# Kernel optimization log

Measured on AMD Instinct MI355X. Metric: run time of the kernel, lower is better.

## Reference

```python
import jax, jax.numpy as jnp
import numpy as np

B, T, D = 2, 2048, 1024
H = 16
HD = D // H  # 64


def _rope_tables(t_len, hd, dtype=jnp.float32):
    inv_freq = 1.0 / (10000.0 ** (jnp.arange(0, hd, 2, dtype=jnp.float32) / hd))
    freqs = jnp.outer(jnp.arange(t_len, dtype=jnp.float32), inv_freq)  # [T, hd/2]
    emb = jnp.concatenate([freqs, freqs], axis=-1)  # [T, hd]
    return emb.astype(dtype)


def _rotate_half(x):
    x1, x2 = jnp.split(x, 2, axis=-1)
    return jnp.concatenate([-x2, x1], axis=-1)


def setup_inputs() -> dict:
    key = jax.random.key(0)
    k1, k2, k3 = jax.random.split(key, 3)
    x = jax.random.normal(k1, (B, T, D), dtype=jnp.float32)
    w_qkv = jax.random.normal(k2, (D, 3 * D), dtype=jnp.float32) * (D ** -0.5)
    w_out = jax.random.normal(k3, (D, D), dtype=jnp.float32) * (D ** -0.5)
    return {"x": x, "w_qkv": w_qkv, "w_out": w_out}


def reference(x, w_qkv, w_out):
    Bc, Tc, Dc = x.shape
    scale = HD ** -0.5
    qkv = x @ w_qkv  # [B,T,3D]
    q, k, v = jnp.split(qkv, 3, axis=-1)
    # -> [B,H,T,hd]
    q = q.reshape(Bc, Tc, H, HD).transpose(0, 2, 1, 3)
    k = k.reshape(Bc, Tc, H, HD).transpose(0, 2, 1, 3)
    v = v.reshape(Bc, Tc, H, HD).transpose(0, 2, 1, 3)
    emb = _rope_tables(Tc, HD, x.dtype)  # [T,hd]
    cos = jnp.cos(emb)[None, None, :, :]
    sin = jnp.sin(emb)[None, None, :, :]
    q = q * cos + _rotate_half(q) * sin
    k = k * cos + _rotate_half(k) * sin
    attn = jnp.einsum('bhqd,bhkd->bhqk', q, k) * scale  # [B,H,T,T]
    causal = jnp.tril(jnp.ones((Tc, Tc), dtype=bool))
    attn = jnp.where(causal[None, None], attn, -jnp.inf)
    attn = jax.nn.softmax(attn, axis=-1)
    out = jnp.einsum('bhqk,bhkd->bhqd', attn, v)
    out = out.transpose(0, 2, 1, 3).reshape(Bc, Tc, Dc)
    return out @ w_out
```

## Files before the change

### kernel.cpp

```cpp
#include <hip/hip_runtime.h>

#define TSEQ 2048
#define DMODEL 1024
#define NHEAD 16
#define HDIM 64
#define NB 2
#define MROWS 4096
#define NQKV 3072
#define QSCALE 0.1803368801111204f
#define ROPE_C (13.2877123795494f / 32.0f)
#define NEGINF -3.0e38f

using s16x8 = __attribute__((ext_vector_type(8))) short;
using s16x4 = __attribute__((ext_vector_type(4))) short;
using f32x4 = __attribute__((ext_vector_type(4))) float;
using u32x2 = __attribute__((ext_vector_type(2))) unsigned int;

static __device__ __forceinline__ float b2f(unsigned short u) {
  union { unsigned int i; float f; } x; x.i = ((unsigned int)u) << 16; return x.f;
}
static __device__ __forceinline__ unsigned short f2b(float f) {
  unsigned int u = __float_as_uint(f);
  u += 0x7fffu + ((u >> 16) & 1u);
  return (unsigned short)(u >> 16);
}

typedef const __attribute__((address_space(1))) char gchar;
typedef __attribute__((address_space(3))) char lchar;
static __device__ __forceinline__ void gload_lds16(const void* g, void* l) {
  __builtin_amdgcn_global_load_lds((gchar*)g, (lchar*)l, 16, 0, 0);
}

__global__ __launch_bounds__(256) void k_prep(const float* __restrict__ x,
                                              short* __restrict__ xb,
                                              const float* __restrict__ wq,
                                              short* __restrict__ wqT,
                                              const float* __restrict__ wo,
                                              short* __restrict__ woT) {
  __shared__ float tile[32][33];
  const int blk = blockIdx.x;
  const int tid = threadIdx.x;
  if (blk < 4096) {
    const int i = blk * 256 + tid;
    const float4 v = ((const float4*)x)[i];
    s16x4 o;
    o.x = (short)f2b(v.x); o.y = (short)f2b(v.y);
    o.z = (short)f2b(v.z); o.w = (short)f2b(v.w);
    ((s16x4*)xb)[i] = o;
    return;
  }
  const float* in; short* out; int C, bx, by;
  if (blk < 7168) {
    const int l = blk - 4096; in = wq; out = wqT; C = NQKV;
    bx = l % 96; by = l / 96;
  } else {
    const int l = blk - 7168; in = wo; out = woT; C = DMODEL;
    bx = l & 31; by = l >> 5;
  }
  const int tx = tid & 31, ty4 = (tid >> 5) * 4;
#pragma unroll
  for (int i = 0; i < 4; ++i)
    tile[ty4 + i][tx] = in[(by * 32 + ty4 + i) * C + bx * 32 + tx];
  __syncthreads();
#pragma unroll
  for (int i = 0; i < 4; ++i)
    out[(bx * 32 + ty4 + i) * DMODEL + by * 32 + tx] = (short)f2b(tile[tx][ty4 + i]);
}

__global__ __launch_bounds__(256) void k_gemm_qkv(const short* __restrict__ A,
                                                  const short* __restrict__ BT,
                                                  short* __restrict__ Qo,
                                                  short* __restrict__ Ko,
                                                  short* __restrict__ Vt) {
  __shared__ __attribute__((aligned(16))) short As[128 * 64];
  __shared__ __attribute__((aligned(16))) short Bs[128 * 64];
  const int K = DMODEL;
  const int tid = threadIdx.x;
  const int wave = tid >> 6, lane = tid & 63, quad = lane >> 4, l15 = lane & 15;
  const int wm = (wave >> 1) * 64, wn = (wave & 1) * 64;
  const int m0 = blockIdx.y * 128, n0 = blockIdx.x * 128;
  f32x4 acc[4][4] = {};
  const char* Ab = (const char*)A;
  const char* Bb = (const char*)BT;
  char* AsB = (char*)As;
  char* BsB = (char*)Bs;
  int srow[4], sg[4];
#pragma unroll
  for (int p = 0; p < 4; ++p) {
    const int i = p * 256 + tid;
    srow[p] = i >> 3;
    sg[p] = (i & 7) ^ (srow[p] & 7);
  }
  for (int k0 = 0; k0 < K; k0 += 64) {
    __syncthreads();
#pragma unroll
    for (int p = 0; p < 4; ++p) {
      const long go = ((long)(m0 + srow[p]) * K + k0) * 2 + sg[p] * 16;
      gload_lds16(Ab + go, AsB + p * 4096 + wave * 1024);
    }
#pragma unroll
    for (int p = 0; p < 4; ++p) {
      const long go = ((long)(n0 + srow[p]) * K + k0) * 2 + sg[p] * 16;
      gload_lds16(Bb + go, BsB + p * 4096 + wave * 1024);
    }
    __syncthreads();
#pragma unroll
    for (int hf = 0; hf < 2; ++hf) {
      s16x8 af[4], bf[4];
#pragma unroll
      for (int i = 0; i < 4; ++i) {
        const int ra = wm + i * 16 + l15;
        af[i] = *(const s16x8*)(AsB + ra * 128 + (((hf * 4 + quad) ^ (ra & 7)) * 16));
        const int rb = wn + i * 16 + l15;
        bf[i] = *(const s16x8*)(BsB + rb * 128 + (((hf * 4 + quad) ^ (rb & 7)) * 16));
      }
#pragma unroll
      for (int i = 0; i < 4; ++i)
#pragma unroll
        for (int j = 0; j < 4; ++j)
          acc[i][j] = __builtin_amdgcn_mfma_f32_16x16x32_bf16(af[i], bf[j], acc[i][j], 0, 0, 0);
    }
  }
  const int colbase = n0 + wn;
  const int region = colbase >> 10;
  const int hh = (colbase & 1023) >> 6;
  const int bq = m0 >> 11;
  const int tbase = (m0 & 2047) + wm;
  if (region == 2) {
    short* dst = Vt + (((long)(bq * NHEAD + hh) * HDIM) << 11);
#pragma unroll
    for (int i = 0; i < 4; ++i) {
      const int t0 = tbase + i * 16 + quad * 4;
#pragma unroll
      for (int j = 0; j < 4; ++j) {
        const int d = j * 16 + l15;
        s16x4 w;
        w.x = (short)f2b(acc[i][j][0]);
        w.y = (short)f2b(acc[i][j][1]);
        w.z = (short)f2b(acc[i][j][2]);
        w.w = (short)f2b(acc[i][j][3]);
        *(s16x4*)(dst + (((long)d) << 11) + t0) = w;
      }
    }
  } else {
    short* dst = (region ? Ko : Qo) + (long)(bq * NHEAD + hh) * TSEQ * HDIM;
#pragma unroll
    for (int i = 0; i < 4; ++i)
#pragma unroll
      for (int j = 0; j < 4; ++j) {
        const int d = j * 16 + l15;
#pragma unroll
        for (int r = 0; r < 4; ++r) {
          const int t = tbase + i * 16 + quad * 4 + r;
          dst[(long)t * HDIM + d] = (short)f2b(acc[i][j][r]);
        }
      }
  }
}

__global__ __launch_bounds__(256) void k_ropek(short* __restrict__ Kp) {
  const int tt = blockIdx.x, bh = blockIdx.y;
  const int tid = threadIdx.x;
  const int row = tid >> 2, chunk = tid & 3;
  const int t = tt * 64 + row;
  short* base = Kp + ((long)bh * TSEQ + t) * HDIM + chunk * 8;
  const s16x8 lo = *(const s16x8*)base;
  const s16x8 hi = *(const s16x8*)(base + 32);
  s16x8 nlo, nhi;
  const float tf = (float)t;
#pragma unroll
  for (int j = 0; j < 8; ++j) {
    const float inv = exp2f(-(float)(chunk * 8 + j) * ROPE_C);
    float sn, cs;
    __sincosf(tf * inv, &sn, &cs);
    const float a = b2f((unsigned short)lo[j]);
    const float b = b2f((unsigned short)hi[j]);
    nlo[j] = (short)f2b(a * cs - b * sn);
    nhi[j] = (short)f2b(b * cs + a * sn);
  }
  *(s16x8*)base = nlo;
  *(s16x8*)(base + 32) = nhi;
}

template <int IM, bool OUT_BF16>
__global__ __launch_bounds__(256) void k_gemm(const short* __restrict__ A,
                                              const short* __restrict__ BT,
                                              void* __restrict__ Cv,
                                              int M, int N, int K) {
  __shared__ __attribute__((aligned(16))) short As[IM * 32 * 64];
  __shared__ __attribute__((aligned(16))) short Bs[128 * 64];
  const int tid = threadIdx.x;
  const int wave = tid >> 6, lane = tid & 63, quad = lane >> 4, l15 = lane & 15;
  const int wm = (wave >> 1) * (IM * 16), wn = (wave & 1) * 64;
  const int m0 = blockIdx.y * (IM * 32), n0 = blockIdx.x * 128;
  f32x4 acc[IM][4] = {};
  const char* Ab = (const char*)A;
  const char* Bb = (const char*)BT;
  char* AsB = (char*)As;
  char* BsB = (char*)Bs;
  int srow[4], sg[4];
#pragma unroll
  for (int p = 0; p < 4; ++p) {
    const int i = p * 256 + tid;
    srow[p] = i >> 3;
    sg[p] = (i & 7) ^ (srow[p] & 7);
  }
  for (int k0 = 0; k0 < K; k0 += 64) {
    __syncthreads();
#pragma unroll
    for (int p = 0; p < IM; ++p) {
      const long go = ((long)(m0 + srow[p]) * K + k0) * 2 + sg[p] * 16;
      gload_lds16(Ab + go, AsB + p * 4096 + wave * 1024);
    }
#pragma unroll
    for (int p = 0; p < 4; ++p) {
      const long go = ((long)(n0 + srow[p]) * K + k0) * 2 + sg[p] * 16;
      gload_lds16(Bb + go, BsB + p * 4096 + wave * 1024);
    }
    __syncthreads();
#pragma unroll
    for (int hf = 0; hf < 2; ++hf) {
      s16x8 af[IM], bf[4];
#pragma unroll
      for (int i = 0; i < IM; ++i) {
        const int ra = wm + i * 16 + l15;
        af[i] = *(const s16x8*)(AsB + ra * 128 + (((hf * 4 + quad) ^ (ra & 7)) * 16));
      }
#pragma unroll
      for (int j = 0; j < 4; ++j) {
        const int rb = wn + j * 16 + l15;
        bf[j] = *(const s16x8*)(BsB + rb * 128 + (((hf * 4 + quad) ^ (rb & 7)) * 16));
      }
#pragma unroll
      for (int i = 0; i < IM; ++i)
#pragma unroll
        for (int j = 0; j < 4; ++j)
          acc[i][j] = __builtin_amdgcn_mfma_f32_16x16x32_bf16(af[i], bf[j], acc[i][j], 0, 0, 0);
    }
  }
#pragma unroll
  for (int i = 0; i < IM; ++i) {
    const int row = m0 + wm + i * 16 + quad * 4;
#pragma unroll
    for (int j = 0; j < 4; ++j) {
      const int col = n0 + wn + j * 16 + l15;
#pragma unroll
      for (int r = 0; r < 4; ++r) {
        if (OUT_BF16) ((short*)Cv)[(long)(row + r) * N + col] = (short)f2b(acc[i][j][r]);
        else          ((float*)Cv)[(long)(row + r) * N + col] = acc[i][j][r];
      }
    }
  }
}

__global__ __launch_bounds__(512) __attribute__((amdgpu_waves_per_eu(4)))
void k_attn(const short* __restrict__ Qg,
            const short* __restrict__ Kg,
            const short* __restrict__ Vg,
            short* __restrict__ O) {
  __shared__ __attribute__((aligned(16))) short Ks[2][64 * 64];
  __shared__ __attribute__((aligned(16))) short Vs[2][64 * 64];
  __shared__ __attribute__((aligned(16))) short pl[8][16 * 64];
  const int bx = blockIdx.x, by = blockIdx.y;
  const int qi = ((by >> 4) & 1) ? (15 - bx) : bx;
  const int bh = by;
  const int b = bh >> 4, h = bh & 15;
  const int tid = threadIdx.x, wave = tid >> 6, lane = tid & 63;
  const int quad = lane >> 4, l15 = lane & 15;
  const char* Kb = (const char*)(Kg + (long)bh * TSEQ * HDIM);
  const char* Vb = (const char*)(Vg + (long)bh * HDIM * TSEQ);
  const short* Qb = Qg + (long)bh * TSEQ * HDIM;
  const int qr0 = qi * 128 + wave * 16;
  const s16x8 rq0 = *(const s16x8*)&Qb[(qr0 + l15) * HDIM + quad * 8];
  const s16x8 rq1 = *(const s16x8*)&Qb[(qr0 + l15) * HDIM + 32 + quad * 8];
  s16x8 aq0, aq1;
  {
    const float tf = (float)(qr0 + l15);
#pragma unroll
    for (int j = 0; j < 8; ++j) {
      const float inv = exp2f(-(float)(quad * 8 + j) * ROPE_C);
      float sn, cs;
      __sincosf(tf * inv, &sn, &cs);
      sn *= QSCALE; cs *= QSCALE;
      const float q0 = b2f((unsigned short)rq0[j]);
      const float q1 = b2f((unsigned short)rq1[j]);
      aq0[j] = (short)f2b(q0 * cs - q1 * sn);
      aq1[j] = (short)f2b(q1 * cs + q0 * sn);
    }
  }
  f32x4 o[4] = {};
  float lsum = 0.0f;
  const int kr0 = tid >> 3, kg0 = (tid & 7) ^ (kr0 & 7);
  char* KsB = (char*)Ks;
  char* VsB = (char*)Vs;
  char* plwB = (char*)pl + wave * 2048;
  const int ldsw = wave * 1024;

#define STAGE(kjv, buf)                                                     \
  do {                                                                      \
    gload_lds16(Kb + (kjv) * 8192 + (kr0 * 8 + kg0) * 16,                   \
                KsB + (buf) * 8192 + ldsw);                                 \
    gload_lds16(Vb + (kjv) * 128 + kr0 * (TSEQ * 2) + kg0 * 16,             \
                VsB + (buf) * 8192 + ldsw);                                 \
  } while (0)

  STAGE(0, 0);
  __syncthreads();

  const int kjmax = 2 * qi + 1;
  const int kjd = qr0 >> 6;
  for (int kj = 0; kj <= kjmax; ++kj) {
    const int cur = kj & 1;
    if (kj < kjmax) STAGE(kj + 1, cur ^ 1);
    if (kj <= kjd) {
      const char* kb = KsB + cur * 8192;
      const char* vb = VsB + cur * 8192;
      f32x4 s[4];
#pragma unroll
      for (int j2 = 0; j2 < 4; ++j2) {
        const int row = j2 * 16 + l15;
        const s16x8 k0 = *(const s16x8*)(kb + row * 128 + ((quad ^ (row & 7)) * 16));
        const s16x8 k1 = *(const s16x8*)(kb + row * 128 + (((4 + quad) ^ (row & 7)) * 16));
        f32x4 z = {};
        z = __builtin_amdgcn_mfma_f32_16x16x32_bf16(k0, aq0, z, 0, 0, 0);
        z = __builtin_amdgcn_mfma_f32_16x16x32_bf16(k1, aq1, z, 0, 0, 0);
        s[j2] = z;
      }
      if (kj == kjd) {
        const int qloc = (qr0 & 63) + l15;
#pragma unroll
        for (int j2 = 0; j2 < 4; ++j2)
#pragma unroll
          for (int r = 0; r < 4; ++r)
            if (j2 * 16 + quad * 4 + r > qloc) s[j2][r] = NEGINF;
      }
      float ps = 0.0f;
#pragma unroll
      for (int j2 = 0; j2 < 4; ++j2) {
        const unsigned int u0 = __float_as_uint(exp2f(s[j2][0])) & 0xffff0000u;
        const unsigned int u1 = __float_as_uint(exp2f(s[j2][1])) & 0xffff0000u;
        const unsigned int u2 = __float_as_uint(exp2f(s[j2][2])) & 0xffff0000u;
        const unsigned int u3 = __float_as_uint(exp2f(s[j2][3])) & 0xffff0000u;
        ps += __uint_as_float(u0) + __uint_as_float(u1) +
              __uint_as_float(u2) + __uint_as_float(u3);
        u32x2 w;
        w.x = (u0 >> 16) | u1;
        w.y = (u2 >> 16) | u3;
        const int t0 = j2 * 16 + quad * 4;
        *(u32x2*)(plwB + l15 * 128 + (((t0 >> 3) ^ (l15 & 7)) * 16) + (quad & 1) * 8) = w;
      }
      lsum += ps;
      const s16x8 bp0 = *(const s16x8*)(plwB + l15 * 128 + ((quad ^ (l15 & 7)) * 16));
      const s16x8 bp1 = *(const s16x8*)(plwB + l15 * 128 + (((4 + quad) ^ (l15 & 7)) * 16));
#pragma unroll
      for (int hs = 0; hs < 4; ++hs) {
        const int d = hs * 16 + l15;
        const s16x8 av0 = *(const s16x8*)(vb + d * 128 + ((quad ^ (d & 7)) * 16));
        const s16x8 av1 = *(const s16x8*)(vb + d * 128 + (((4 + quad) ^ (d & 7)) * 16));
        o[hs] = __builtin_amdgcn_mfma_f32_16x16x32_bf16(av0, bp0, o[hs], 0, 0, 0);
        o[hs] = __builtin_amdgcn_mfma_f32_16x16x32_bf16(av1, bp1, o[hs], 0, 0, 0);
      }
    }
    __syncthreads();
  }
#undef STAGE
  lsum += __shfl_xor(lsum, 16);
  lsum += __shfl_xor(lsum, 32);
  const float rinv = 1.0f / lsum;
  const int t = qr0 + l15;
  short* Orow = O + (long)(b * TSEQ + t) * DMODEL + h * HDIM + quad * 4;
#pragma unroll
  for (int hs = 0; hs < 4; ++hs) {
    s16x4 w;
    w.x = (short)f2b(o[hs][0] * rinv);
    w.y = (short)f2b(o[hs][1] * rinv);
    w.z = (short)f2b(o[hs][2] * rinv);
    w.w = (short)f2b(o[hs][3] * rinv);
    *(s16x4*)(Orow + hs * 16) = w;
  }
}

extern "C" void kernel_launch(void* const* d_in, const int* in_sizes, int n_in,
                              void* d_out, int out_size, void* d_ws, size_t ws_size,
                              hipStream_t stream) {
  const float* x = (const float*)d_in[0];
  const float* w_qkv = (const float*)d_in[1];
  const float* w_out = (const float*)d_in[2];
  float* out = (float*)d_out;
  char* ws = (char*)d_ws;

  short* xb    = (short*)(ws);
  short* wqkvT = (short*)(ws + (8ll << 20));
  short* woutT = (short*)(ws + (14ll << 20));
  short* Qb    = (short*)(ws + (16ll << 20));
  short* Kb    = (short*)(ws + (24ll << 20));
  short* Vt    = (short*)(ws + (32ll << 20));
  short* Ob    = (short*)(ws + (40ll << 20));

  k_prep<<<dim3(8192), dim3(256), 0, stream>>>(x, xb, w_qkv, wqkvT, w_out, woutT);
  k_gemm_qkv<<<dim3(NQKV / 128, MROWS / 128), dim3(256), 0, stream>>>(
      xb, wqkvT, Qb, Kb, Vt);
  k_ropek<<<dim3(TSEQ / 64, NB * NHEAD), dim3(256), 0, stream>>>(Kb);
  k_attn<<<dim3(TSEQ / 128, NB * NHEAD), dim3(512), 0, stream>>>(Qb, Kb, Vt, Ob);
  k_gemm<2, false><<<dim3(DMODEL / 128, MROWS / 64), dim3(256), 0, stream>>>(
      Ob, woutT, (void*)out, MROWS, DMODEL, DMODEL);
}
```

Measured before the change: 192.5 us.

## Give each attention wave two 16-row query tiles and halve the block size

The attention kernel now runs 4 waves per block instead of 8, and each wave owns 32 query rows split into two 16-row subtiles. Each K and V fragment read from LDS feeds twice as many MFMAs, which cuts LDS read traffic per unit of work. The K/V tile staging is split across two loads per thread to match the smaller block. In exchange, register pressure roughly doubles for the accumulators (waves_per_eu lowered to 2). The causal skip is also coarser: a wave keeps processing key blocks up to the diagonal of its last row, which adds some wasted work for the first subtile.

```diff
diff --git a/kernel.cpp b/kernel.cpp
--- a/kernel.cpp
+++ b/kernel.cpp
@@ -253,14 +253,14 @@
   }
 }
 
-__global__ __launch_bounds__(512) __attribute__((amdgpu_waves_per_eu(4)))
+__global__ __launch_bounds__(256) __attribute__((amdgpu_waves_per_eu(2)))
 void k_attn(const short* __restrict__ Qg,
             const short* __restrict__ Kg,
             const short* __restrict__ Vg,
             short* __restrict__ O) {
   __shared__ __attribute__((aligned(16))) short Ks[2][64 * 64];
   __shared__ __attribute__((aligned(16))) short Vs[2][64 * 64];
-  __shared__ __attribute__((aligned(16))) short pl[8][16 * 64];
+  __shared__ __attribute__((aligned(16))) short pl[4][2][16 * 64];
   const int bx = blockIdx.x, by = blockIdx.y;
   const int qi = ((by >> 4) & 1) ? (15 - bx) : bx;
   const int bh = by;
@@ -270,12 +270,14 @@
   const char* Kb = (const char*)(Kg + (long)bh * TSEQ * HDIM);
   const char* Vb = (const char*)(Vg + (long)bh * HDIM * TSEQ);
   const short* Qb = Qg + (long)bh * TSEQ * HDIM;
-  const int qr0 = qi * 128 + wave * 16;
-  const s16x8 rq0 = *(const s16x8*)&Qb[(qr0 + l15) * HDIM + quad * 8];
-  const s16x8 rq1 = *(const s16x8*)&Qb[(qr0 + l15) * HDIM + 32 + quad * 8];
-  s16x8 aq0, aq1;
-  {
-    const float tf = (float)(qr0 + l15);
+  const int qw0 = qi * 128 + wave * 32;
+  s16x8 aq[2][2];
+#pragma unroll
+  for (int qh = 0; qh < 2; ++qh) {
+    const int qrow = qw0 + qh * 16 + l15;
+    const s16x8 rq0 = *(const s16x8*)&Qb[qrow * HDIM + quad * 8];
+    const s16x8 rq1 = *(const s16x8*)&Qb[qrow * HDIM + 32 + quad * 8];
+    const float tf = (float)qrow;
 #pragma unroll
     for (int j = 0; j < 8; ++j) {
       const float inv = exp2f(-(float)(quad * 8 + j) * ROPE_C);
@@ -284,99 +286,122 @@
       sn *= QSCALE; cs *= QSCALE;
       const float q0 = b2f((unsigned short)rq0[j]);
       const float q1 = b2f((unsigned short)rq1[j]);
-      aq0[j] = (short)f2b(q0 * cs - q1 * sn);
-      aq1[j] = (short)f2b(q1 * cs + q0 * sn);
-    }
-  }
-  f32x4 o[4] = {};
-  float lsum = 0.0f;
+      aq[qh][0][j] = (short)f2b(q0 * cs - q1 * sn);
+      aq[qh][1][j] = (short)f2b(q1 * cs + q0 * sn);
+    }
+  }
+  f32x4 o[2][4] = {};
+  float lsum[2] = {0.0f, 0.0f};
   const int kr0 = tid >> 3, kg0 = (tid & 7) ^ (kr0 & 7);
+  const int kr1 = (tid + 256) >> 3, kg1 = (tid & 7) ^ (kr1 & 7);
   char* KsB = (char*)Ks;
   char* VsB = (char*)Vs;
-  char* plwB = (char*)pl + wave * 2048;
-  const int ldsw = wave * 1024;
+  char* plwB = (char*)pl + wave * 4096;
+  const int ldsw0 = wave * 1024, ldsw1 = 4096 + wave * 1024;
 
 #define STAGE(kjv, buf)                                                     \
   do {                                                                      \
-    gload_lds16(Kb + (kjv) * 8192 + (kr0 * 8 + kg0) * 16,                   \
-                KsB + (buf) * 8192 + ldsw);                                 \
-    gload_lds16(Vb + (kjv) * 128 + kr0 * (TSEQ * 2) + kg0 * 16,             \
-                VsB + (buf) * 8192 + ldsw);                                 \
+    const char* Kt_ = Kb + (kjv) * 8192;                                    \
+    const char* Vt_ = Vb + (kjv) * 128;                                     \
+    char* kd_ = KsB + (buf) * 8192;                                         \
+    char* vd_ = VsB + (buf) * 8192;                                         \
+    gload_lds16(Kt_ + (kr0 * 8 + kg0) * 16, kd_ + ldsw0);                   \
+    gload_lds16(Kt_ + (kr1 * 8 + kg1) * 16, kd_ + ldsw1);                   \
+    gload_lds16(Vt_ + kr0 * (TSEQ * 2) + kg0 * 16, vd_ + ldsw0);            \
+    gload_lds16(Vt_ + kr1 * (TSEQ * 2) + kg1 * 16, vd_ + ldsw1);            \
   } while (0)
 
   STAGE(0, 0);
   __syncthreads();
 
   const int kjmax = 2 * qi + 1;
-  const int kjd = qr0 >> 6;
+  const int kjd = (qw0 + 31) >> 6;
   for (int kj = 0; kj <= kjmax; ++kj) {
     const int cur = kj & 1;
     if (kj < kjmax) STAGE(kj + 1, cur ^ 1);
     if (kj <= kjd) {
       const char* kb = KsB + cur * 8192;
       const char* vb = VsB + cur * 8192;
-      f32x4 s[4];
+      f32x4 s[2][4];
 #pragma unroll
       for (int j2 = 0; j2 < 4; ++j2) {
         const int row = j2 * 16 + l15;
         const s16x8 k0 = *(const s16x8*)(kb + row * 128 + ((quad ^ (row & 7)) * 16));
         const s16x8 k1 = *(const s16x8*)(kb + row * 128 + (((4 + quad) ^ (row & 7)) * 16));
-        f32x4 z = {};
-        z = __builtin_amdgcn_mfma_f32_16x16x32_bf16(k0, aq0, z, 0, 0, 0);
-        z = __builtin_amdgcn_mfma_f32_16x16x32_bf16(k1, aq1, z, 0, 0, 0);
-        s[j2] = z;
+#pragma unroll
+        for (int qh = 0; qh < 2; ++qh) {
+          f32x4 z = {};
+          z = __builtin_amdgcn_mfma_f32_16x16x32_bf16(k0, aq[qh][0], z, 0, 0, 0);
+          z = __builtin_amdgcn_mfma_f32_16x16x32_bf16(k1, aq[qh][1], z, 0, 0, 0);
+          s[qh][j2] = z;
+        }
       }
       if (kj == kjd) {
-        const int qloc = (qr0 & 63) + l15;
-#pragma unroll
-        for (int j2 = 0; j2 < 4; ++j2)
-#pragma unroll
-          for (int r = 0; r < 4; ++r)
-            if (j2 * 16 + quad * 4 + r > qloc) s[j2][r] = NEGINF;
-      }
-      float ps = 0.0f;
-#pragma unroll
-      for (int j2 = 0; j2 < 4; ++j2) {
-        const unsigned int u0 = __float_as_uint(exp2f(s[j2][0])) & 0xffff0000u;
-        const unsigned int u1 = __float_as_uint(exp2f(s[j2][1])) & 0xffff0000u;
-        const unsigned int u2 = __float_as_uint(exp2f(s[j2][2])) & 0xffff0000u;
-        const unsigned int u3 = __float_as_uint(exp2f(s[j2][3])) & 0xffff0000u;
-        ps += __uint_as_float(u0) + __uint_as_float(u1) +
-              __uint_as_float(u2) + __uint_as_float(u3);
-        u32x2 w;
-        w.x = (u0 >> 16) | u1;
-        w.y = (u2 >> 16) | u3;
-        const int t0 = j2 * 16 + quad * 4;
-        *(u32x2*)(plwB + l15 * 128 + (((t0 >> 3) ^ (l15 & 7)) * 16) + (quad & 1) * 8) = w;
-      }
-      lsum += ps;
-      const s16x8 bp0 = *(const s16x8*)(plwB + l15 * 128 + ((quad ^ (l15 & 7)) * 16));
-      const s16x8 bp1 = *(const s16x8*)(plwB + l15 * 128 + (((4 + quad) ^ (l15 & 7)) * 16));
+#pragma unroll
+        for (int qh = 0; qh < 2; ++qh) {
+          const int qloc = (qw0 & 63) + qh * 16 + l15;
+#pragma unroll
+          for (int j2 = 0; j2 < 4; ++j2)
+#pragma unroll
+            for (int r = 0; r < 4; ++r)
+              if (j2 * 16 + quad * 4 + r > qloc) s[qh][j2][r] = NEGINF;
+        }
+      }
+#pragma unroll
+      for (int qh = 0; qh < 2; ++qh) {
+        float ps = 0.0f;
+#pragma unroll
+        for (int j2 = 0; j2 < 4; ++j2) {
+          const unsigned int u0 = __float_as_uint(exp2f(s[qh][j2][0])) & 0xffff0000u;
+          const unsigned int u1 = __float_as_uint(exp2f(s[qh][j2][1])) & 0xffff0000u;
+          const unsigned int u2 = __float_as_uint(exp2f(s[qh][j2][2])) & 0xffff0000u;
+          const unsigned int u3 = __float_as_uint(exp2f(s[qh][j2][3])) & 0xffff0000u;
+          ps += __uint_as_float(u0) + __uint_as_float(u1) +
+                __uint_as_float(u2) + __uint_as_float(u3);
+          u32x2 w;
+          w.x = (u0 >> 16) | u1;
+          w.y = (u2 >> 16) | u3;
+          const int t0 = j2 * 16 + quad * 4;
+          *(u32x2*)(plwB + qh * 2048 + l15 * 128 +
+                    (((t0 >> 3) ^ (l15 & 7)) * 16) + (quad & 1) * 8) = w;
+        }
+        lsum[qh] += ps;
+      }
+      const s16x8 bp00 = *(const s16x8*)(plwB + l15 * 128 + ((quad ^ (l15 & 7)) * 16));
+      const s16x8 bp01 = *(const s16x8*)(plwB + l15 * 128 + (((4 + quad) ^ (l15 & 7)) * 16));
+      const s16x8 bp10 = *(const s16x8*)(plwB + 2048 + l15 * 128 + ((quad ^ (l15 & 7)) * 16));
+      const s16x8 bp11 = *(const s16x8*)(plwB + 2048 + l15 * 128 + (((4 + quad) ^ (l15 & 7)) * 16));
 #pragma unroll
       for (int hs = 0; hs < 4; ++hs) {
         const int d = hs * 16 + l15;
         const s16x8 av0 = *(const s16x8*)(vb + d * 128 + ((quad ^ (d & 7)) * 16));
         const s16x8 av1 = *(const s16x8*)(vb + d * 128 + (((4 + quad) ^ (d & 7)) * 16));
-        o[hs] = __builtin_amdgcn_mfma_f32_16x16x32_bf16(av0, bp0, o[hs], 0, 0, 0);
-        o[hs] = __builtin_amdgcn_mfma_f32_16x16x32_bf16(av1, bp1, o[hs], 0, 0, 0);
+        o[0][hs] = __builtin_amdgcn_mfma_f32_16x16x32_bf16(av0, bp00, o[0][hs], 0, 0, 0);
+        o[0][hs] = __builtin_amdgcn_mfma_f32_16x16x32_bf16(av1, bp01, o[0][hs], 0, 0, 0);
+        o[1][hs] = __builtin_amdgcn_mfma_f32_16x16x32_bf16(av0, bp10, o[1][hs], 0, 0, 0);
+        o[1][hs] = __builtin_amdgcn_mfma_f32_16x16x32_bf16(av1, bp11, o[1][hs], 0, 0, 0);
       }
     }
     __syncthreads();
   }
 #undef STAGE
-  lsum += __shfl_xor(lsum, 16);
-  lsum += __shfl_xor(lsum, 32);
-  const float rinv = 1.0f / lsum;
-  const int t = qr0 + l15;
-  short* Orow = O + (long)(b * TSEQ + t) * DMODEL + h * HDIM + quad * 4;
-#pragma unroll
-  for (int hs = 0; hs < 4; ++hs) {
-    s16x4 w;
-    w.x = (short)f2b(o[hs][0] * rinv);
-    w.y = (short)f2b(o[hs][1] * rinv);
-    w.z = (short)f2b(o[hs][2] * rinv);
-    w.w = (short)f2b(o[hs][3] * rinv);
-    *(s16x4*)(Orow + hs * 16) = w;
+#pragma unroll
+  for (int qh = 0; qh < 2; ++qh) {
+    float ls = lsum[qh];
+    ls += __shfl_xor(ls, 16);
+    ls += __shfl_xor(ls, 32);
+    const float rinv = 1.0f / ls;
+    const int t = qw0 + qh * 16 + l15;
+    short* Orow = O + (long)(b * TSEQ + t) * DMODEL + h * HDIM + quad * 4;
+#pragma unroll
+    for (int hs = 0; hs < 4; ++hs) {
+      s16x4 w;
+      w.x = (short)f2b(o[qh][hs][0] * rinv);
+      w.y = (short)f2b(o[qh][hs][1] * rinv);
+      w.z = (short)f2b(o[qh][hs][2] * rinv);
+      w.w = (short)f2b(o[qh][hs][3] * rinv);
+      *(s16x4*)(Orow + hs * 16) = w;
+    }
   }
 }
 
@@ -401,7 +426,7 @@
   k_gemm_qkv<<<dim3(NQKV / 128, MROWS / 128), dim3(256), 0, stream>>>(
       xb, wqkvT, Qb, Kb, Vt);
   k_ropek<<<dim3(TSEQ / 64, NB * NHEAD), dim3(256), 0, stream>>>(Kb);
-  k_attn<<<dim3(TSEQ / 128, NB * NHEAD), dim3(512), 0, stream>>>(Qb, Kb, Vt, Ob);
+  k_attn<<<dim3(TSEQ / 128, NB * NHEAD), dim3(256), 0, stream>>>(Qb, Kb, Vt, Ob);
   k_gemm<2, false><<<dim3(DMODEL / 128, MROWS / 64), dim3(256), 0, stream>>>(
       Ob, woutT, (void*)out, MROWS, DMODEL, DMODEL);
 }
```

New measurement: 197.8 us. +2.7%, slower.
